# Kernel optimization log

Hardware: AMD Instinct MI355X
Metric: run time of the kernel (lower is better)

## Reference

```python
import jax, jax.numpy as jnp
import numpy as np
import math

SR = 24000
NH = 100      # num_harmonics
NF = 5        # num_formants
HID = 128
TWO_PI = 2.0 * math.pi


def conv1d(x, w, b, groups=1):
    # x: [B,C,T], w: [O, C//groups, K] (torch OIH layout), 'same' padding
    pad = (w.shape[-1] - 1) // 2
    y = jax.lax.conv_general_dilated(
        x, w, window_strides=(1,), padding=[(pad, pad)],
        dimension_numbers=('NCH', 'OIH', 'NCH'), feature_group_count=groups)
    return y + b[None, :, None]


def lrelu(x):
    return jnp.where(x >= 0, x, 0.1 * x)


def interp_linear(x, L):
    # torch F.interpolate(mode='linear', align_corners=False): x [B,C,T] -> [B,C,L]
    B, C, T = x.shape
    pos = (jnp.arange(L, dtype=x.dtype) + 0.5) * (T / L) - 0.5
    pos = jnp.clip(pos, 0.0, float(T - 1))
    lo = jnp.floor(pos).astype(jnp.int32)
    hi = jnp.minimum(lo + 1, T - 1)
    w = pos - lo.astype(x.dtype)
    return x[:, :, lo] * (1.0 - w) + x[:, :, hi] * w


def setup_inputs():
    key = jax.random.key(0)
    ks = jax.random.split(key, 30)
    ki = iter(range(30))
    def p(shape, s=0.05):
        return s * jax.random.normal(ks[next(ki)], shape, jnp.float32)
    B, T, L = 4, 500, 120000
    inp = {}
    # f0 in [80,120) Hz so actual_harmonics == num_harmonics (static shapes, see notes)
    inp['f0'] = 80.0 + 40.0 * jax.random.uniform(ks[next(ki)], (B, T), jnp.float32)
    inp['condition'] = jax.random.normal(ks[next(ki)], (B, HID, T), jnp.float32)
    # harmonic_amplitude_net params
    inp['ha_w1'] = p((HID, 1, 3));   inp['ha_b1'] = p((HID,))
    inp['ha_w2'] = p((256, HID, 1)); inp['ha_b2'] = p((256,))
    inp['ha_w3'] = p((256, 1, 3));   inp['ha_b3'] = p((256,))
    inp['ha_w4'] = p((256, 256, 1)); inp['ha_b4'] = p((256,))
    inp['ha_w5'] = p((NH, 256, 1));  inp['ha_b5'] = p((NH,))
    # formant predictor params
    inp['fm_w1'] = p((256, HID, 3));    inp['fm_b1'] = p((256,))
    inp['fm_w2'] = p((256, 256, 3));    inp['fm_b2'] = p((256,))
    inp['fm_w3'] = p((2 * NF, 256, 1)); inp['fm_b3'] = p((2 * NF,))
    # voice quality predictor params
    inp['vq_w1'] = p((128, HID, 3)); inp['vq_b1'] = p((128,))
    inp['vq_w2'] = p((64, 128, 3));  inp['vq_b2'] = p((64,))
    inp['vq_w3'] = p((3, 64, 1));    inp['vq_b3'] = p((3,))
    inp['audio_length'] = L
    return inp


def reference(f0, condition,
              ha_w1, ha_b1, ha_w2, ha_b2, ha_w3, ha_b3, ha_w4, ha_b4, ha_w5, ha_b5,
              fm_w1, fm_b1, fm_w2, fm_b2, fm_w3, fm_b3,
              vq_w1, vq_b1, vq_w2, vq_b2, vq_w3, vq_b3,
              audio_length):
    B, T = f0.shape
    L = audio_length
    # ---- harmonic_amplitude_net: (dw3 -> pw1 -> lrelu) x2 -> pw1 -> softplus ----
    a = lrelu(conv1d(conv1d(condition, ha_w1, ha_b1, groups=HID), ha_w2, ha_b2))
    a = lrelu(conv1d(conv1d(a, ha_w3, ha_b3, groups=256), ha_w4, ha_b4))
    harmonic_amplitudes = jax.nn.softplus(conv1d(a, ha_w5, ha_b5))  # [B,NH,T]
    # ---- FormantNetwork ----
    fp = conv1d(lrelu(conv1d(lrelu(conv1d(condition, fm_w1, fm_b1)), fm_w2, fm_b2)), fm_w3, fm_b3)
    ff = 200.0 + 3300.0 * jax.nn.sigmoid(fp[:, :NF])        # [B,NF,T]
    fbw = 50.0 + 150.0 * jax.nn.softplus(fp[:, NF:])        # [B,NF,T]
    hidx = jnp.arange(1, NH + 1, dtype=f0.dtype)
    hfreq = hidx[None, :, None] * f0[:, None, :]            # [B,NH,T]
    num = fbw ** 2                                          # [B,NF,T]
    den = (hfreq[:, None] - ff[:, :, None]) ** 2 + num[:, :, None]  # [B,NF,NH,T]
    res = num[:, :, None] / jnp.maximum(den, 1e-5)
    gain = jnp.prod(0.8 + 0.2 * res, axis=1)                # [B,NH,T]
    shaped = harmonic_amplitudes * gain
    # ---- VoiceQualityNetwork ----
    q = jax.nn.sigmoid(conv1d(lrelu(conv1d(lrelu(conv1d(condition, vq_w1, vq_b1)), vq_w2, vq_b2)), vq_w3, vq_b3))
    q_up = interp_linear(q, L)                              # [B,3,L]
    jitter = q_up[:, 0] * 0.05
    shimmer = q_up[:, 1] * 0.15
    breath = q_up[:, 2] * 0.3
    # ---- phase integration + harmonic bank ----
    f0_up = interp_linear(f0[:, None, :], L)[:, 0]          # [B,L]
    phase = jnp.cumsum(TWO_PI * f0_up / SR, axis=1)
    nk1, nk2, nk3 = jax.random.split(jax.random.key(42), 3)
    jphase = phase + jitter * jax.random.normal(nk1, phase.shape, phase.dtype)
    mask = (hidx[None, :, None] * f0_up[:, None, :] < SR / 2).astype(f0.dtype)  # [B,NH,L]
    amps_up = interp_linear(shaped, L)                      # [B,NH,L]
    sig = jnp.sum(amps_up * jnp.sin(jphase[:, None, :] * hidx[None, :, None]) * mask, axis=1)
    # ---- voice qualities: shimmer envelope + breath noise ----
    shim_env = 1.0 + jax.random.normal(nk2, sig.shape, sig.dtype) * shimmer
    out = sig * shim_env + jax.random.normal(nk3, sig.shape, sig.dtype) * breath
    return out
```

## Files before the change

### kernel.cpp

```cpp
#include <hip/hip_runtime.h>
#include <stdint.h>

#define B_ 4
#define T_ 500
#define L_ 120000
#define NH_ 100
#define N1_ 7500
#define N2_ 469
#define N2P_ 7504
#define N3_ 30
#define N3P_ 480
#define N4_ 2
#define N4P_ 32

#define ACT_NONE 0
#define ACT_LRELU 1
#define ACT_SOFTPLUS 2
#define ACT_SIGMOID 3

#define CH3 32
#define SXW3 132

__host__ __device__ __forceinline__ uint32_t tf_rotl(uint32_t v, int d) {
  return (v << d) | (v >> (32 - d));
}
__host__ __device__ __forceinline__ void tf_block(uint32_t k0, uint32_t k1,
                                                  uint32_t& x0, uint32_t& x1) {
  uint32_t k2 = k0 ^ k1 ^ 0x1BD11BDAu;
  x0 += k0; x1 += k1;
#define TF_R(d) x0 += x1; x1 = tf_rotl(x1, (d)); x1 ^= x0;
  TF_R(13) TF_R(15) TF_R(26) TF_R(6)   x0 += k1; x1 += k2 + 1u;
  TF_R(17) TF_R(29) TF_R(16) TF_R(24)  x0 += k2; x1 += k0 + 2u;
  TF_R(13) TF_R(15) TF_R(26) TF_R(6)   x0 += k0; x1 += k1 + 3u;
  TF_R(17) TF_R(29) TF_R(16) TF_R(24)  x0 += k1; x1 += k2 + 4u;
  TF_R(13) TF_R(15) TF_R(26) TF_R(6)   x0 += k2; x1 += k0 + 5u;
#undef TF_R
}

__device__ __forceinline__ float erfinv_xla(float x) {
  float w = -log1pf(-(x * x));
  float p;
  if (w < 5.0f) {
    w = w - 2.5f;
    p = 2.81022636e-08f;
    p = fmaf(p, w, 3.43273939e-07f);
    p = fmaf(p, w, -3.5233877e-06f);
    p = fmaf(p, w, -4.39150654e-06f);
    p = fmaf(p, w, 0.00021858087f);
    p = fmaf(p, w, -0.00125372503f);
    p = fmaf(p, w, -0.00417768164f);
    p = fmaf(p, w, 0.246640727f);
    p = fmaf(p, w, 1.50140941f);
  } else {
    w = sqrtf(w) - 3.0f;
    p = -0.000200214257f;
    p = fmaf(p, w, 0.000100950558f);
    p = fmaf(p, w, 0.00134934322f);
    p = fmaf(p, w, -0.00367342844f);
    p = fmaf(p, w, 0.00573950773f);
    p = fmaf(p, w, -0.0076224613f);
    p = fmaf(p, w, 0.00943887047f);
    p = fmaf(p, w, 1.00167406f);
    p = fmaf(p, w, 2.83297682f);
  }
  return p * x;
}

__device__ __forceinline__ float jax_normal(uint32_t k0, uint32_t k1, uint32_t e) {
  uint32_t x0 = 0u, x1 = e;
  tf_block(k0, k1, x0, x1);
  uint32_t bits = x0 ^ x1;
  float u = __uint_as_float((bits >> 9) | 0x3f800000u) - 1.0f;
  float v = __fadd_rn(__fmul_rn(u, 2.0f), -0x1.fffffep-1f);
  v = fmaxf(v, -0x1.fffffep-1f);
  return __fmul_rn((float)1.4142135623730951, erfinv_xla(v));
}

__device__ __forceinline__ float sin_acc(float xf) {
  double x = (double)xf;
  double kd = rint(x * 6.3661977236758138e-01);
  double r = fma(-kd, 1.5707963267948966e+00, x);
  r = fma(-kd, 6.1232339957367660e-17, r);
  float rf = (float)r;
  float y = rf * rf;
  float ps = fmaf(y, 2.7557319e-06f, -1.9841270e-04f);
  ps = fmaf(y, ps, 8.3333335e-03f);
  ps = fmaf(y, ps, -0.16666667f);
  float s = fmaf(rf * y, ps, rf);
  float pc = fmaf(y, -2.7557319e-07f, 2.4801587e-05f);
  pc = fmaf(y, pc, -1.3888889e-03f);
  pc = fmaf(y, pc, 4.1666668e-02f);
  pc = fmaf(y, pc, -0.5f);
  float c = fmaf(y, pc, 1.0f);
  int q = ((int)kd) & 3;
  float rs = (q & 1) ? c : s;
  return (q & 2) ? -rs : rs;
}

__device__ __forceinline__ float apply_act(float v, int act) {
  switch (act) {
    case ACT_LRELU:    return v >= 0.0f ? v : 0.1f * v;
    case ACT_SOFTPLUS: return fmaxf(v, 0.0f) + log1pf(expf(-fabsf(v)));
    case ACT_SIGMOID:  return 1.0f / (1.0f + expf(-v));
  }
  return v;
}


__device__ __forceinline__ void conv3_tile(
    const float* __restrict__ x, const float* __restrict__ w,
    const float* __restrict__ bias, float* __restrict__ y,
    int Cin, int Cout, int o0, int act, int b, int t0, float* smem) {
  float* sxf = smem;
  float* swf = smem + CH3 * SXW3;
  int tid = threadIdx.x;
  int lane = tid & 63, og = tid >> 6;
  int tl = 2 * lane;
  int t = t0 + tl;
  int obase = o0 + og * 4;
  float acc[4][2];
#pragma unroll
  for (int i = 0; i < 4; ++i) {
    float bv = (obase + i < Cout) ? bias[obase + i] : 0.0f;
    acc[i][0] = bv; acc[i][1] = bv;
  }
  float rx[17], rw[6];
  const int nch = Cin / CH3;
  auto ld = [&](int c) {
    int cb = c * CH3;
#pragma unroll
    for (int k = 0; k < 17; ++k) {
      int idx = tid + 256 * k;
      float v = 0.0f;
      if (idx < CH3 * 130) {
        int cc = idx / 130, j = idx - cc * 130;
        int tt = t0 - 1 + j;
        if (tt >= 0 && tt < T_) v = x[((size_t)b * Cin + cb + cc) * T_ + tt];
      }
      rx[k] = v;
    }
#pragma unroll
    for (int k = 0; k < 6; ++k) {
      int idx = tid + 256 * k;
      int oo = idx / 96, r = idx - oo * 96;
      rw[k] = (o0 + oo < Cout) ? w[((size_t)(o0 + oo) * Cin + cb) * 3 + r] : 0.0f;
    }
  };
  ld(0);
  for (int c = 0; c < nch; ++c) {
    __syncthreads();
#pragma unroll
    for (int k = 0; k < 17; ++k) {
      int idx = tid + 256 * k;
      if (idx < CH3 * 130) {
        int cc = idx / 130, j = idx - cc * 130;
        sxf[cc * SXW3 + j] = rx[k];
      }
    }
#pragma unroll
    for (int k = 0; k < 6; ++k) {
      int idx = tid + 256 * k;
      int oo = idx / 96, r = idx - oo * 96;
      swf[(r / 3) * 52 + oo * 3 + (r % 3)] = rw[k];
    }
    __syncthreads();
    if (c + 1 < nch) ld(c + 1);
    for (int cc = 0; cc < CH3; ++cc) {
      const float* row = sxf + cc * SXW3 + tl;
      float2 xa = *(const float2*)row;
      float2 xb = *(const float2*)(row + 2);
      const float4* wq = (const float4*)(swf + cc * 52 + og * 12);
      float4 W0 = wq[0], W1 = wq[1], W2 = wq[2];
      float wl[12] = {W0.x, W0.y, W0.z, W0.w, W1.x, W1.y, W1.z, W1.w,
                      W2.x, W2.y, W2.z, W2.w};
#pragma unroll
      for (int i = 0; i < 4; ++i) {
        float w0 = wl[3 * i], w1 = wl[3 * i + 1], w2 = wl[3 * i + 2];
        acc[i][0] = fmaf(xa.x, w0, acc[i][0]);
        acc[i][0] = fmaf(xa.y, w1, acc[i][0]);
        acc[i][0] = fmaf(xb.x, w2, acc[i][0]);
        acc[i][1] = fmaf(xa.y, w0, acc[i][1]);
        acc[i][1] = fmaf(xb.x, w1, acc[i][1]);
        acc[i][1] = fmaf(xb.y, w2, acc[i][1]);
      }
    }
  }
#pragma unroll
  for (int i = 0; i < 4; ++i) {
    int o = obase + i;
    if (o < Cout) {
      if (t < T_)     y[((size_t)b * Cout + o) * T_ + t]     = apply_act(acc[i][0], act);
      if (t + 1 < T_) y[((size_t)b * Cout + o) * T_ + t + 1] = apply_act(acc[i][1], act);
    }
  }
}

__device__ __forceinline__ void dwpw_tile(
    const float* __restrict__ x, const float* __restrict__ wd,
    const float* __restrict__ bd, const float* __restrict__ wp,
    const float* __restrict__ bp, float* __restrict__ y,
    int Cin, int Cout, int o0, int act, int b, int t0, float* smem) {
  float* sxf  = smem;
  float* swdf = smem + CH3 * SXW3;
  float* swpf = swdf + CH3 * 4;
  int tid = threadIdx.x;
  int lane = tid & 63, og = tid >> 6;
  int tl = 2 * lane;
  int t = t0 + tl;
  int obase = o0 + og * 4;
  float acc[4][2];
#pragma unroll
  for (int i = 0; i < 4; ++i) {
    float bv = (obase + i < Cout) ? bp[obase + i] : 0.0f;
    acc[i][0] = bv; acc[i][1] = bv;
  }
  float rx[17], rwp[2], rwd1 = 0.0f;
  const int nch = Cin / CH3;
  auto ld = [&](int c) {
    int cb = c * CH3;
#pragma unroll
    for (int k = 0; k < 17; ++k) {
      int idx = tid + 256 * k;
      float v = 0.0f;
      if (idx < CH3 * 130) {
        int cc = idx / 130, j = idx - cc * 130;
        int tt = t0 - 1 + j;
        if (tt >= 0 && tt < T_) v = x[((size_t)b * Cin + cb + cc) * T_ + tt];
      }
      rx[k] = v;
    }
    if (tid < CH3 * 4) {
      int cc = tid >> 2, q = tid & 3;
      rwd1 = (q < 3) ? wd[(size_t)(cb + cc) * 3 + q] : bd[cb + cc];
    }
#pragma unroll
    for (int k = 0; k < 2; ++k) {
      int idx = tid + 256 * k;
      int oo = idx >> 5, cc = idx & 31;
      rwp[k] = (o0 + oo < Cout) ? wp[(size_t)(o0 + oo) * Cin + cb + cc] : 0.0f;
    }
  };
  ld(0);
  for (int c = 0; c < nch; ++c) {
    __syncthreads();
#pragma unroll
    for (int k = 0; k < 17; ++k) {
      int idx = tid + 256 * k;
      if (idx < CH3 * 130) {
        int cc = idx / 130, j = idx - cc * 130;
        sxf[cc * SXW3 + j] = rx[k];
      }
    }
    if (tid < CH3 * 4) swdf[tid] = rwd1;
#pragma unroll
    for (int k = 0; k < 2; ++k) {
      int idx = tid + 256 * k;
      int oo = idx >> 5, cc = idx & 31;
      swpf[cc * 16 + oo] = rwp[k];
    }
    __syncthreads();
    if (c + 1 < nch) ld(c + 1);
    for (int cc = 0; cc < CH3; ++cc) {
      const float* row = sxf + cc * SXW3 + tl;
      float2 xa = *(const float2*)row;
      float2 xb = *(const float2*)(row + 2);
      float4 D = *(const float4*)(swdf + cc * 4);
      float d0 = fmaf(xa.x, D.x, fmaf(xa.y, D.y, fmaf(xb.x, D.z, D.w)));
      float d1 = fmaf(xa.y, D.x, fmaf(xb.x, D.y, fmaf(xb.y, D.z, D.w)));
      float4 Wp = *(const float4*)(swpf + cc * 16 + og * 4);
      acc[0][0] = fmaf(d0, Wp.x, acc[0][0]);
      acc[1][0] = fmaf(d0, Wp.y, acc[1][0]);
      acc[2][0] = fmaf(d0, Wp.z, acc[2][0]);
      acc[3][0] = fmaf(d0, Wp.w, acc[3][0]);
      acc[0][1] = fmaf(d1, Wp.x, acc[0][1]);
      acc[1][1] = fmaf(d1, Wp.y, acc[1][1]);
      acc[2][1] = fmaf(d1, Wp.z, acc[2][1]);
      acc[3][1] = fmaf(d1, Wp.w, acc[3][1]);
    }
  }
#pragma unroll
  for (int i = 0; i < 4; ++i) {
    int o = obase + i;
    if (o < Cout) {
      if (t < T_)     y[((size_t)b * Cout + o) * T_ + t]     = apply_act(acc[i][0], act);
      if (t + 1 < T_) y[((size_t)b * Cout + o) * T_ + t + 1] = apply_act(acc[i][1], act);
    }
  }
}

__device__ __forceinline__ void pw_stream(
    const float* __restrict__ x, const float* __restrict__ w,
    const float* __restrict__ bias, float* __restrict__ y,
    int Cin, int Cout, int o0, int act, int b, int t0, float* smem) {
  for (int idx = threadIdx.x; idx < 16 * Cin; idx += 256) {
    int oo = idx / Cin, cc = idx - oo * Cin;
    smem[cc * 16 + oo] = (o0 + oo < Cout) ? w[(size_t)(o0 + oo) * Cin + cc] : 0.0f;
  }
  __syncthreads();
  int lane = threadIdx.x & 63, og = threadIdx.x >> 6;
  int t = t0 + lane;
  int obase = o0 + og * 4;
  float acc[4];
#pragma unroll
  for (int i = 0; i < 4; ++i)
    acc[i] = (obase + i < Cout) ? bias[obase + i] : 0.0f;
  if (t < T_) {
    const float* xr = x + (size_t)b * Cin * T_ + t;
#pragma unroll 4
    for (int cc = 0; cc < Cin; ++cc) {
      float xv = xr[(size_t)cc * T_];
      float4 Wp = *(const float4*)(smem + cc * 16 + og * 4);
      acc[0] = fmaf(xv, Wp.x, acc[0]);
      acc[1] = fmaf(xv, Wp.y, acc[1]);
      acc[2] = fmaf(xv, Wp.z, acc[2]);
      acc[3] = fmaf(xv, Wp.w, acc[3]);
    }
#pragma unroll
    for (int i = 0; i < 4; ++i) {
      int o = obase + i;
      if (o < Cout) y[((size_t)b * Cout + o) * T_ + t] = apply_act(acc[i], act);
    }
  }
}

__device__ void terms_body(const float* __restrict__ f0, float* __restrict__ A1,
                           int base, int stride) {
  const float RINV = (float)(500.0 / 120000.0);
  for (int gid = base; gid < B_ * N1_; gid += stride) {
    int b = gid / N1_, w = gid - b * N1_;
    const float* f0b = f0 + (size_t)b * T_;
    float* a = A1 + (size_t)b * L_ + (size_t)w * 16;
    float S = 0.0f;
    int lbase = w * 16;
    for (int i = 0; i < 16; ++i) {
      int l = lbase + i;
      float pos = __fsub_rn(__fmul_rn(__fadd_rn((float)l, 0.5f), RINV), 0.5f);
      pos = fminf(fmaxf(pos, 0.0f), 499.0f);
      int lo = (int)floorf(pos);
      int hi = lo + 1; hi = hi < (T_ - 1) ? hi : (T_ - 1);
      float wt = __fsub_rn(pos, (float)lo);
      float omw = __fsub_rn(1.0f, wt);
      float f0up = __fadd_rn(__fmul_rn(f0b[lo], omw), __fmul_rn(f0b[hi], wt));
      float trm = __fdiv_rn(__fmul_rn((float)6.283185307179586, f0up), 24000.0f);
      S = __fadd_rn(S, trm);
      a[i] = S;
    }
  }
}

__device__ void rwr_body(const float* __restrict__ A1, float* __restrict__ A2,
                         float* __restrict__ A3, float* __restrict__ A4,
                         float* __restrict__ E5, float* __restrict__ E3o,
                         float* __restrict__ E2o) {
  int tid = threadIdx.x;
  for (int gid = tid; gid < B_ * N2_; gid += 256) {
    int b = gid / N2_, w = gid - b * N2_;
    float S = 0.0f;
    for (int m = 0; m < 16; ++m) {
      int i = w * 16 + m;
      float v = (i < N1_) ? A1[(size_t)b * L_ + (size_t)i * 16 + 15] : 0.0f;
      S = __fadd_rn(S, v);
      A2[(size_t)b * N2P_ + i] = S;
    }
  }
  __syncthreads();
  for (int gid = tid; gid < B_ * N3_; gid += 256) {
    int b = gid / N3_, w = gid - b * N3_;
    float S = 0.0f;
    for (int m = 0; m < 16; ++m) {
      int i = w * 16 + m;
      float v = (i < N2_) ? A2[(size_t)b * N2P_ + (size_t)i * 16 + 15] : 0.0f;
      S = __fadd_rn(S, v);
      A3[(size_t)b * N3P_ + i] = S;
    }
  }
  __syncthreads();
  for (int gid = tid; gid < B_ * N4_; gid += 256) {
    int b = gid / N4_, w = gid - b * N4_;
    float S = 0.0f;
    for (int m = 0; m < 16; ++m) {
      int i = w * 16 + m;
      float v = (i < N3_) ? A3[(size_t)b * N3P_ + (size_t)i * 16 + 15] : 0.0f;
      S = __fadd_rn(S, v);
      A4[(size_t)b * N4P_ + i] = S;
    }
  }
  __syncthreads();
  if (tid < B_) {
    E5[tid * N4_ + 0] = 0.0f;
    E5[tid * N4_ + 1] = A4[(size_t)tid * N4P_ + 15];
  }
  __syncthreads();
  for (int gid = tid; gid < B_ * N3_; gid += 256) {
    int b = gid / N3_, k = gid - b * N3_;
    float v = 0.0f;
    if (k > 0) {
      int i = k - 1;
      v = __fadd_rn(E5[b * N4_ + (i >> 4)], A4[(size_t)b * N4P_ + i]);
    }
    E3o[b * N3_ + k] = v;
  }
  __syncthreads();
  for (int gid = tid; gid < B_ * N2_; gid += 256) {
    int b = gid / N2_, j = gid - b * N2_;
    float v = 0.0f;
    if (j > 0) {
      int i = j - 1;
      v = __fadd_rn(E3o[b * N3_ + (i >> 4)], A3[(size_t)b * N3P_ + i]);
    }
    E2o[b * N2_ + j] = v;
  }
}

__global__ void __launch_bounds__(256) conv_l1(
    const float* __restrict__ cond, const float* __restrict__ f0,
    const float* __restrict__ fw1, const float* __restrict__ fb1,
    const float* __restrict__ vw1, const float* __restrict__ vb1,
    const float* __restrict__ hw1, const float* __restrict__ hb1,
    const float* __restrict__ hw2, const float* __restrict__ hb2,
    float* __restrict__ fmA, float* __restrict__ vqB, float* __restrict__ haB,
    float* __restrict__ A1) {
  __shared__ __align__(16) float smem[CH3 * SXW3 + CH3 * 52];
  int yy = blockIdx.y, b = blockIdx.z, t0 = blockIdx.x * 128;
  if (yy < 16) {
    conv3_tile(cond, fw1, fb1, fmA, 128, 256, yy * 16, ACT_LRELU, b, t0, smem);
  } else if (yy < 24) {
    conv3_tile(cond, vw1, vb1, vqB, 128, 128, (yy - 16) * 16, ACT_LRELU, b, t0, smem);
  } else if (yy < 40) {
    dwpw_tile(cond, hw1, hb1, hw2, hb2, haB, 128, 256, (yy - 24) * 16, ACT_LRELU, b, t0, smem);
  } else {
    int base = (blockIdx.z * 4 + blockIdx.x) * 256 + threadIdx.x;
    terms_body(f0, A1, base, 4096);
  }
}

__global__ void __launch_bounds__(256) conv_l2(
    const float* __restrict__ fmA, const float* __restrict__ vqB,
    const float* __restrict__ haB,
    const float* __restrict__ fw2, const float* __restrict__ fb2,
    const float* __restrict__ vw2, const float* __restrict__ vb2,
    const float* __restrict__ hw3, const float* __restrict__ hb3,
    const float* __restrict__ hw4, const float* __restrict__ hb4,
    float* __restrict__ fmC, float* __restrict__ vqC, float* __restrict__ haC,
    const float* __restrict__ A1, float* __restrict__ A2, float* __restrict__ A3,
    float* __restrict__ A4, float* __restrict__ E5, float* __restrict__ E3o,
    float* __restrict__ E2o) {
  __shared__ __align__(16) float smem[CH3 * SXW3 + CH3 * 52];
  int yy = blockIdx.y, b = blockIdx.z, t0 = blockIdx.x * 128;
  if (yy < 16) {
    conv3_tile(fmA, fw2, fb2, fmC, 256, 256, yy * 16, ACT_LRELU, b, t0, smem);
  } else if (yy < 20) {
    conv3_tile(vqB, vw2, vb2, vqC, 128, 64, (yy - 16) * 16, ACT_LRELU, b, t0, smem);
  } else if (yy < 36) {
    dwpw_tile(haB, hw3, hb3, hw4, hb4, haC, 256, 256, (yy - 20) * 16, ACT_LRELU, b, t0, smem);
  } else {
    if (blockIdx.x != 0 || blockIdx.z != 0) return;
    rwr_body(A1, A2, A3, A4, E5, E3o, E2o);
  }
}

__global__ void __launch_bounds__(256) conv_l3(
    const float* __restrict__ haC, const float* __restrict__ fmC,
    const float* __restrict__ vqC,
    const float* __restrict__ hw5, const float* __restrict__ hb5,
    const float* __restrict__ fw3, const float* __restrict__ fb3,
    const float* __restrict__ vw3, const float* __restrict__ vb3,
    float* __restrict__ ha, float* __restrict__ fp, float* __restrict__ qv) {
  __shared__ __align__(16) float smem[4096];
  int yy = blockIdx.y, b = blockIdx.z, t0 = blockIdx.x * 64;
  if (yy < 7) {
    pw_stream(haC, hw5, hb5, ha, 256, 100, yy * 16, ACT_SOFTPLUS, b, t0, smem);
  } else if (yy == 7) {
    pw_stream(fmC, fw3, fb3, fp, 256, 10, 0, ACT_NONE, b, t0, smem);
  } else {
    pw_stream(vqC, vw3, vb3, qv, 64, 3, 0, ACT_SIGMOID, b, t0, smem);
  }
}

__global__ void __launch_bounds__(256) main_kernel(
    const float* __restrict__ A1, const float* __restrict__ A2,
    const float* __restrict__ E2o,
    const float* __restrict__ ha, const float* __restrict__ fp,
    const float* __restrict__ q,
    const float* __restrict__ f0, float* __restrict__ out,
    uint32_t k10, uint32_t k11, uint32_t k20, uint32_t k21, uint32_t k30, uint32_t k31) {
  const float RINV = (float)(500.0 / 120000.0);
  int b = blockIdx.y;
  int l0 = blockIdx.x * 256;
  int l = l0 + threadIdx.x;
  __shared__ float ls[4][NH_];
  __shared__ float sff[4][5], snm[4][5];
  float p0 = __fsub_rn(__fmul_rn(__fadd_rn((float)l0, 0.5f), RINV), 0.5f);
  p0 = fminf(fmaxf(p0, 0.0f), 499.0f);
  int lo0 = (int)floorf(p0);
  if (threadIdx.x < 40) {
    int j = threadIdx.x / 10, h = threadIdx.x - j * 10;
    int col = lo0 + j; col = col < (T_ - 1) ? col : (T_ - 1);
    float v = fp[((size_t)b * 10 + h) * T_ + col];
    if (h < 5) {
      sff[j][h] = 200.0f + 3300.0f * (1.0f / (1.0f + expf(-v)));
    } else {
      float bw = 50.0f + 150.0f * (fmaxf(v, 0.0f) + log1pf(expf(-fabsf(v))));
      snm[j][h - 5] = bw * bw;
    }
  }
  __syncthreads();
  for (int i = threadIdx.x; i < 4 * NH_; i += 256) {
    int j = i / NH_, h = i - j * NH_;
    int col = lo0 + j; col = col < (T_ - 1) ? col : (T_ - 1);
    float hfreq = (float)(h + 1) * f0[(size_t)b * T_ + col];
    float g = 1.0f;
    for (int ii = 0; ii < 5; ++ii) {
      float d = hfreq - sff[j][ii];
      float den = d * d + snm[j][ii];
      float res = snm[j][ii] / fmaxf(den, 1e-5f);
      g = g * (0.8f + 0.2f * res);
    }
    ls[j][h] = ha[((size_t)b * NH_ + h) * T_ + col] * g;
  }
  __syncthreads();
  if (l >= L_) return;

  float pos = __fsub_rn(__fmul_rn(__fadd_rn((float)l, 0.5f), RINV), 0.5f);
  pos = fminf(fmaxf(pos, 0.0f), 499.0f);
  int lo = (int)floorf(pos);
  int hi = lo + 1; hi = hi < (T_ - 1) ? hi : (T_ - 1);
  float w = __fsub_rn(pos, (float)lo);
  float omw = __fsub_rn(1.0f, w);

  const float* f0b = f0 + (size_t)b * T_;
  float f0up = __fadd_rn(__fmul_rn(f0b[lo], omw), __fmul_rn(f0b[hi], w));
  const float* qb = q + (size_t)b * 3 * T_;
  float q0 = __fadd_rn(__fmul_rn(qb[lo], omw), __fmul_rn(qb[hi], w));
  float q1 = __fadd_rn(__fmul_rn(qb[T_ + lo], omw), __fmul_rn(qb[T_ + hi], w));
  float q2 = __fadd_rn(__fmul_rn(qb[2 * T_ + lo], omw), __fmul_rn(qb[2 * T_ + hi], w));
  float jit = __fmul_rn(q0, 0.05f);
  float shm = __fmul_rn(q1, 0.15f);
  float brt = __fmul_rn(q2, 0.3f);

  uint32_t e = (uint32_t)(b * L_ + l);
  float n1 = jax_normal(k10, k11, e);
  float n2 = jax_normal(k20, k21, e);
  float n3 = jax_normal(k30, k31, e);

  float e1v = 0.0f;
  int r = l >> 4;
  if (r > 0) {
    int i = r - 1;
    e1v = __fadd_rn(E2o[b * N2_ + (i >> 4)], A2[(size_t)b * N2P_ + i]);
  }
  float phf = __fadd_rn(e1v, A1[(size_t)b * L_ + l]);
  float jph = __fadd_rn(phf, __fmul_rn(jit, n1));

  int jlo = lo - lo0;
  int jhi = hi - lo0; jhi = jhi < 3 ? jhi : 3;

  float acc = 0.0f;
  for (int h = 1; h <= NH_; ++h) {
    float amp = __fadd_rn(__fmul_rn(ls[jlo][h - 1], omw), __fmul_rn(ls[jhi][h - 1], w));
    float hf = (float)h;
    float arg = __fmul_rn(jph, hf);
    float s = sin_acc(arg);
    float m = (__fmul_rn(hf, f0up) < 12000.0f) ? 1.0f : 0.0f;
    acc = __fadd_rn(acc, __fmul_rn(__fmul_rn(amp, s), m));
  }
  float env = __fadd_rn(1.0f, __fmul_rn(n2, shm));
  out[(size_t)b * L_ + l] = __fadd_rn(__fmul_rn(acc, env), __fmul_rn(n3, brt));
}

extern "C" void kernel_launch(void* const* d_in, const int* in_sizes, int n_in,
                              void* d_out, int out_size, void* d_ws, size_t ws_size,
                              hipStream_t stream) {
  const float* f0    = (const float*)d_in[0];
  const float* cond  = (const float*)d_in[1];
  const float* ha_w1 = (const float*)d_in[2];
  const float* ha_b1 = (const float*)d_in[3];
  const float* ha_w2 = (const float*)d_in[4];
  const float* ha_b2 = (const float*)d_in[5];
  const float* ha_w3 = (const float*)d_in[6];
  const float* ha_b3 = (const float*)d_in[7];
  const float* ha_w4 = (const float*)d_in[8];
  const float* ha_b4 = (const float*)d_in[9];
  const float* ha_w5 = (const float*)d_in[10];
  const float* ha_b5 = (const float*)d_in[11];
  const float* fm_w1 = (const float*)d_in[12];
  const float* fm_b1 = (const float*)d_in[13];
  const float* fm_w2 = (const float*)d_in[14];
  const float* fm_b2 = (const float*)d_in[15];
  const float* fm_w3 = (const float*)d_in[16];
  const float* fm_b3 = (const float*)d_in[17];
  const float* vq_w1 = (const float*)d_in[18];
  const float* vq_b1 = (const float*)d_in[19];
  const float* vq_w2 = (const float*)d_in[20];
  const float* vq_b2 = (const float*)d_in[21];
  const float* vq_w3 = (const float*)d_in[22];
  const float* vq_b3 = (const float*)d_in[23];
  float* out = (float*)d_out;

  uint32_t kw[3][2];
  for (uint32_t j = 0; j < 3; ++j) {
    uint32_t x0 = 0u, x1 = j;
    tf_block(0u, 42u, x0, x1);
    kw[j][0] = x0; kw[j][1] = x1;
  }

  float* ws = (float*)d_ws;
  size_t off = 0;
  auto take = [&](size_t n) { float* p = ws + off; off += (n + 3) & ~(size_t)3; return p; };
  float* fmA = take(512000);
  float* haB = take(512000);
  float* fmC = take(512000);
  float* haC = take(512000);
  float* vqB = take(256000);
  float* vqC = take(128000);
  float* A1  = take((size_t)B_ * L_);
  float* A2  = take((size_t)B_ * N2P_);
  float* A3  = take((size_t)B_ * N3P_);
  float* A4  = take((size_t)B_ * N4P_);
  float* E5  = take((size_t)B_ * N4_);
  float* E3o = take((size_t)B_ * N3_);
  float* E2o = take((size_t)B_ * N2_);
  float* ha = fmA;
  float* fp = vqB;
  float* qv = vqB + 20480;

  conv_l1<<<dim3(4, 41, B_), 256, 0, stream>>>(
      cond, f0, fm_w1, fm_b1, vq_w1, vq_b1, ha_w1, ha_b1, ha_w2, ha_b2,
      fmA, vqB, haB, A1);
  conv_l2<<<dim3(4, 37, B_), 256, 0, stream>>>(
      fmA, vqB, haB, fm_w2, fm_b2, vq_w2, vq_b2, ha_w3, ha_b3, ha_w4, ha_b4,
      fmC, vqC, haC, A1, A2, A3, A4, E5, E3o, E2o);
  conv_l3<<<dim3(8, 9, B_), 256, 0, stream>>>(
      haC, fmC, vqC, ha_w5, ha_b5, fm_w3, fm_b3, vq_w3, vq_b3, ha, fp, qv);
  main_kernel<<<dim3((L_ + 255) / 256, B_), 256, 0, stream>>>(
      A1, A2, E2o, ha, fp, qv, f0, out,
      kw[0][0], kw[0][1], kw[1][0], kw[1][1], kw[2][0], kw[2][1]);
  (void)in_sizes; (void)n_in; (void)out_size; (void)ws_size;
}
```

Before: 275.1 us.

## Stage conv tiles via async global-to-LDS loads with double buffering

The 3-tap and depthwise+pointwise conv tiles used to stage inputs and weights through registers and then write them to shared memory. They now issue direct global-to-LDS loads (global_load_lds) into a double-buffered shared-memory layout. Out-of-range elements read from a zeroed scratch buffer, and only one barrier per channel chunk remains. The aim is to remove register pressure and the LDS write step, and to overlap loading the next chunk with compute. In exchange, shared memory per block roughly doubles, which may lower occupancy, and correctness depends on the async loads being waited on before the barrier.

```diff
diff --git a/kernel.cpp b/kernel.cpp
--- a/kernel.cpp
+++ b/kernel.cpp
@@ -19,7 +19,12 @@
 #define ACT_SIGMOID 3
 
 #define CH3 32
-#define SXW3 132
+#define XN 4352
+#define WN 1536
+#define BUFA (XN + WN)
+
+typedef const __attribute__((address_space(1))) void* gp1_t;
+typedef __attribute__((address_space(3))) void* lp3_t;
 
 __host__ __device__ __forceinline__ uint32_t tf_rotl(uint32_t v, int d) {
   return (v << d) | (v >> (32 - d));
@@ -107,12 +112,11 @@
 }
 
 
-__device__ __forceinline__ void conv3_tile(
+__device__ __forceinline__ void conv3_async(
     const float* __restrict__ x, const float* __restrict__ w,
     const float* __restrict__ bias, float* __restrict__ y,
+    const float* __restrict__ zbuf,
     int Cin, int Cout, int o0, int act, int b, int t0, float* smem) {
-  float* sxf = smem;
-  float* swf = smem + CH3 * SXW3;
   int tid = threadIdx.x;
   int lane = tid & 63, og = tid >> 6;
   int tl = 2 * lane;
@@ -124,52 +128,42 @@
     float bv = (obase + i < Cout) ? bias[obase + i] : 0.0f;
     acc[i][0] = bv; acc[i][1] = bv;
   }
-  float rx[17], rw[6];
   const int nch = Cin / CH3;
-  auto ld = [&](int c) {
+  auto issue = [&](int c, float* buf) {
     int cb = c * CH3;
 #pragma unroll
     for (int k = 0; k < 17; ++k) {
       int idx = tid + 256 * k;
-      float v = 0.0f;
+      const float* src = zbuf;
       if (idx < CH3 * 130) {
         int cc = idx / 130, j = idx - cc * 130;
         int tt = t0 - 1 + j;
-        if (tt >= 0 && tt < T_) v = x[((size_t)b * Cin + cb + cc) * T_ + tt];
+        if (tt >= 0 && tt < T_) src = x + ((size_t)b * Cin + cb + cc) * T_ + tt;
       }
-      rx[k] = v;
+      __builtin_amdgcn_global_load_lds((gp1_t)src, (lp3_t)(buf + idx), 4, 0, 0);
     }
 #pragma unroll
     for (int k = 0; k < 6; ++k) {
-      int idx = tid + 256 * k;
-      int oo = idx / 96, r = idx - oo * 96;
-      rw[k] = (o0 + oo < Cout) ? w[((size_t)(o0 + oo) * Cin + cb) * 3 + r] : 0.0f;
+      int p = tid + 256 * k;
+      int cc = p / 48, r = p - cc * 48;
+      int oo = r / 3, kk = r - oo * 3;
+      const float* src = (o0 + oo < Cout)
+          ? w + ((size_t)(o0 + oo) * Cin + cb + cc) * 3 + kk : zbuf;
+      __builtin_amdgcn_global_load_lds((gp1_t)src, (lp3_t)(buf + XN + p), 4, 0, 0);
     }
   };
-  ld(0);
+  issue(0, smem);
   for (int c = 0; c < nch; ++c) {
     __syncthreads();
-#pragma unroll
-    for (int k = 0; k < 17; ++k) {
-      int idx = tid + 256 * k;
-      if (idx < CH3 * 130) {
-        int cc = idx / 130, j = idx - cc * 130;
-        sxf[cc * SXW3 + j] = rx[k];
-      }
-    }
-#pragma unroll
-    for (int k = 0; k < 6; ++k) {
-      int idx = tid + 256 * k;
-      int oo = idx / 96, r = idx - oo * 96;
-      swf[(r / 3) * 52 + oo * 3 + (r % 3)] = rw[k];
-    }
-    __syncthreads();
-    if (c + 1 < nch) ld(c + 1);
+    const float* cur = smem + (c & 1) * BUFA;
+    if (c + 1 < nch) issue(c + 1, smem + ((c + 1) & 1) * BUFA);
+    const float* sxf = cur;
+    const float* swf = cur + XN;
     for (int cc = 0; cc < CH3; ++cc) {
-      const float* row = sxf + cc * SXW3 + tl;
+      const float* row = sxf + cc * 130 + tl;
       float2 xa = *(const float2*)row;
       float2 xb = *(const float2*)(row + 2);
-      const float4* wq = (const float4*)(swf + cc * 52 + og * 12);
+      const float4* wq = (const float4*)(swf + cc * 48 + og * 12);
       float4 W0 = wq[0], W1 = wq[1], W2 = wq[2];
       float wl[12] = {W0.x, W0.y, W0.z, W0.w, W1.x, W1.y, W1.z, W1.w,
                       W2.x, W2.y, W2.z, W2.w};
@@ -195,14 +189,12 @@
   }
 }
 
-__device__ __forceinline__ void dwpw_tile(
+__device__ __forceinline__ void dwpw_async(
     const float* __restrict__ x, const float* __restrict__ wd,
     const float* __restrict__ bd, const float* __restrict__ wp,
     const float* __restrict__ bp, float* __restrict__ y,
+    const float* __restrict__ zbuf,
     int Cin, int Cout, int o0, int act, int b, int t0, float* smem) {
-  float* sxf  = smem;
-  float* swdf = smem + CH3 * SXW3;
-  float* swpf = swdf + CH3 * 4;
   int tid = threadIdx.x;
   int lane = tid & 63, og = tid >> 6;
   int tl = 2 * lane;
@@ -214,54 +206,45 @@
     float bv = (obase + i < Cout) ? bp[obase + i] : 0.0f;
     acc[i][0] = bv; acc[i][1] = bv;
   }
-  float rx[17], rwp[2], rwd1 = 0.0f;
   const int nch = Cin / CH3;
-  auto ld = [&](int c) {
+  auto issue = [&](int c, float* buf) {
     int cb = c * CH3;
 #pragma unroll
     for (int k = 0; k < 17; ++k) {
       int idx = tid + 256 * k;
-      float v = 0.0f;
+      const float* src = zbuf;
       if (idx < CH3 * 130) {
         int cc = idx / 130, j = idx - cc * 130;
         int tt = t0 - 1 + j;
-        if (tt >= 0 && tt < T_) v = x[((size_t)b * Cin + cb + cc) * T_ + tt];
+        if (tt >= 0 && tt < T_) src = x + ((size_t)b * Cin + cb + cc) * T_ + tt;
       }
-      rx[k] = v;
-    }
-    if (tid < CH3 * 4) {
-      int cc = tid >> 2, q = tid & 3;
-      rwd1 = (q < 3) ? wd[(size_t)(cb + cc) * 3 + q] : bd[cb + cc];
-    }
-#pragma unroll
-    for (int k = 0; k < 2; ++k) {
-      int idx = tid + 256 * k;
-      int oo = idx >> 5, cc = idx & 31;
-      rwp[k] = (o0 + oo < Cout) ? wp[(size_t)(o0 + oo) * Cin + cb + cc] : 0.0f;
+      __builtin_amdgcn_global_load_lds((gp1_t)src, (lp3_t)(buf + idx), 4, 0, 0);
+    }
+#pragma unroll
+    for (int k = 0; k < 3; ++k) {
+      int p = tid + 256 * k;
+      const float* src = zbuf;
+      if (p < 128) {
+        int cc = p >> 2, q = p & 3;
+        src = (q < 3) ? wd + (size_t)(cb + cc) * 3 + q : bd + cb + cc;
+      } else if (p < 640) {
+        int pp = p - 128;
+        int cc = pp >> 4, oo = pp & 15;
+        if (o0 + oo < Cout) src = wp + (size_t)(o0 + oo) * Cin + cb + cc;
+      }
+      __builtin_amdgcn_global_load_lds((gp1_t)src, (lp3_t)(buf + XN + p), 4, 0, 0);
     }
   };
-  ld(0);
+  issue(0, smem);
   for (int c = 0; c < nch; ++c) {
     __syncthreads();
-#pragma unroll
-    for (int k = 0; k < 17; ++k) {
-      int idx = tid + 256 * k;
-      if (idx < CH3 * 130) {
-        int cc = idx / 130, j = idx - cc * 130;
-        sxf[cc * SXW3 + j] = rx[k];
-      }
-    }
-    if (tid < CH3 * 4) swdf[tid] = rwd1;
-#pragma unroll
-    for (int k = 0; k < 2; ++k) {
-      int idx = tid + 256 * k;
-      int oo = idx >> 5, cc = idx & 31;
-      swpf[cc * 16 + oo] = rwp[k];
-    }
-    __syncthreads();
-    if (c + 1 < nch) ld(c + 1);
+    const float* cur = smem + (c & 1) * BUFA;
+    if (c + 1 < nch) issue(c + 1, smem + ((c + 1) & 1) * BUFA);
+    const float* sxf  = cur;
+    const float* swdf = cur + XN;
+    const float* swpf = cur + XN + 128;
     for (int cc = 0; cc < CH3; ++cc) {
-      const float* row = sxf + cc * SXW3 + tl;
+      const float* row = sxf + cc * 130 + tl;
       float2 xa = *(const float2*)row;
       float2 xb = *(const float2*)(row + 2);
       float4 D = *(const float4*)(swdf + cc * 4);
@@ -419,15 +402,15 @@
     const float* __restrict__ hw1, const float* __restrict__ hb1,
     const float* __restrict__ hw2, const float* __restrict__ hb2,
     float* __restrict__ fmA, float* __restrict__ vqB, float* __restrict__ haB,
-    float* __restrict__ A1) {
-  __shared__ __align__(16) float smem[CH3 * SXW3 + CH3 * 52];
+    float* __restrict__ A1, const float* __restrict__ zbuf) {
+  __shared__ __align__(16) float smem[2 * BUFA];
   int yy = blockIdx.y, b = blockIdx.z, t0 = blockIdx.x * 128;
   if (yy < 16) {
-    conv3_tile(cond, fw1, fb1, fmA, 128, 256, yy * 16, ACT_LRELU, b, t0, smem);
+    conv3_async(cond, fw1, fb1, fmA, zbuf, 128, 256, yy * 16, ACT_LRELU, b, t0, smem);
   } else if (yy < 24) {
-    conv3_tile(cond, vw1, vb1, vqB, 128, 128, (yy - 16) * 16, ACT_LRELU, b, t0, smem);
+    conv3_async(cond, vw1, vb1, vqB, zbuf, 128, 128, (yy - 16) * 16, ACT_LRELU, b, t0, smem);
   } else if (yy < 40) {
-    dwpw_tile(cond, hw1, hb1, hw2, hb2, haB, 128, 256, (yy - 24) * 16, ACT_LRELU, b, t0, smem);
+    dwpw_async(cond, hw1, hb1, hw2, hb2, haB, zbuf, 128, 256, (yy - 24) * 16, ACT_LRELU, b, t0, smem);
   } else {
     int base = (blockIdx.z * 4 + blockIdx.x) * 256 + threadIdx.x;
     terms_body(f0, A1, base, 4096);
@@ -444,15 +427,15 @@
     float* __restrict__ fmC, float* __restrict__ vqC, float* __restrict__ haC,
     const float* __restrict__ A1, float* __restrict__ A2, float* __restrict__ A3,
     float* __restrict__ A4, float* __restrict__ E5, float* __restrict__ E3o,
-    float* __restrict__ E2o) {
-  __shared__ __align__(16) float smem[CH3 * SXW3 + CH3 * 52];
+    float* __restrict__ E2o, const float* __restrict__ zbuf) {
+  __shared__ __align__(16) float smem[2 * BUFA];
   int yy = blockIdx.y, b = blockIdx.z, t0 = blockIdx.x * 128;
   if (yy < 16) {
-    conv3_tile(fmA, fw2, fb2, fmC, 256, 256, yy * 16, ACT_LRELU, b, t0, smem);
+    conv3_async(fmA, fw2, fb2, fmC, zbuf, 256, 256, yy * 16, ACT_LRELU, b, t0, smem);
   } else if (yy < 20) {
-    conv3_tile(vqB, vw2, vb2, vqC, 128, 64, (yy - 16) * 16, ACT_LRELU, b, t0, smem);
+    conv3_async(vqB, vw2, vb2, vqC, zbuf, 128, 64, (yy - 16) * 16, ACT_LRELU, b, t0, smem);
   } else if (yy < 36) {
-    dwpw_tile(haB, hw3, hb3, hw4, hb4, haC, 256, 256, (yy - 20) * 16, ACT_LRELU, b, t0, smem);
+    dwpw_async(haB, hw3, hb3, hw4, hb4, haC, zbuf, 256, 256, (yy - 20) * 16, ACT_LRELU, b, t0, smem);
   } else {
     if (blockIdx.x != 0 || blockIdx.z != 0) return;
     rwr_body(A1, A2, A3, A4, E5, E3o, E2o);
@@ -620,16 +603,19 @@
   float* E5  = take((size_t)B_ * N4_);
   float* E3o = take((size_t)B_ * N3_);
   float* E2o = take((size_t)B_ * N2_);
+  float* zbuf = take(64);
   float* ha = fmA;
   float* fp = vqB;
   float* qv = vqB + 20480;
 
+  hipMemsetAsync(zbuf, 0, 64 * sizeof(float), stream);
+
   conv_l1<<<dim3(4, 41, B_), 256, 0, stream>>>(
       cond, f0, fm_w1, fm_b1, vq_w1, vq_b1, ha_w1, ha_b1, ha_w2, ha_b2,
-      fmA, vqB, haB, A1);
+      fmA, vqB, haB, A1, zbuf);
   conv_l2<<<dim3(4, 37, B_), 256, 0, stream>>>(
       fmA, vqB, haB, fm_w2, fm_b2, vq_w2, vq_b2, ha_w3, ha_b3, ha_w4, ha_b4,
-      fmC, vqC, haC, A1, A2, A3, A4, E5, E3o, E2o);
+      fmC, vqC, haC, A1, A2, A3, A4, E5, E3o, E2o, zbuf);
   conv_l3<<<dim3(8, 9, B_), 256, 0, stream>>>(
       haC, fmC, vqC, ha_w5, ha_b5, fm_w3, fm_b3, vq_w3, vq_b3, ha, fp, qv);
   main_kernel<<<dim3((L_ + 255) / 256, B_), 256, 0, stream>>>(
```

Measured after the change: 276.1 us. No clear change (+0.4%).
